# Optimization experiments

Measured on AMD Instinct MI355X. Metric: run time of the kernel, lower is better.

## Reference

```python
import jax, jax.numpy as jnp
import numpy as np

N_NODES = 50000
N_EDGES = 600000
DIMS = [1280, 512, 300, 300]


def setup_inputs() -> dict:
    key = jax.random.key(0)
    ks = jax.random.split(key, 8)
    x = jax.random.normal(ks[0], (N_NODES, DIMS[0]), dtype=jnp.float32)
    edge_index = jax.random.randint(ks[1], (2, N_EDGES), 0, N_NODES, dtype=jnp.int64)
    def w(k, i, o):
        return jax.random.normal(k, (i, o), dtype=jnp.float32) * (1.0 / np.sqrt(i))
    W1 = w(ks[2], DIMS[0], DIMS[1]); b1 = jnp.zeros((DIMS[1],), jnp.float32)
    W2 = w(ks[3], DIMS[1], DIMS[2]); b2 = jnp.zeros((DIMS[2],), jnp.float32)
    W3 = w(ks[4], DIMS[2], DIMS[3]); b3 = jnp.zeros((DIMS[3],), jnp.float32)
    return {"x": x, "W1": W1, "b1": b1, "W2": W2, "b2": b2,
            "W3": W3, "b3": b3, "edge_index": edge_index}


def gcn_conv(x, W, b, src, dst, n):
    """PyG GCNConv: add self-loops, symmetric D^-1/2 (A+I) D^-1/2 aggregation."""
    h = x @ W  # [N, out]
    loops = jnp.arange(n, dtype=src.dtype)
    s = jnp.concatenate([src, loops])  # [E+N]
    d = jnp.concatenate([dst, loops])
    deg = jax.ops.segment_sum(jnp.ones_like(d, dtype=h.dtype), d, num_segments=n)
    dinv = jnp.where(deg > 0, jax.lax.rsqrt(deg), 0.0)
    norm = dinv[s] * dinv[d]  # [E+N]
    out = jax.ops.segment_sum(h[s] * norm[:, None], d, num_segments=n)
    return out + b


def reference(x, W1, b1, W2, b2, W3, b3, edge_index):
    src, dst = edge_index[0], edge_index[1]
    n = x.shape[0]
    # dropout is identity in eval mode; pertubed=False path
    h = jax.nn.relu(gcn_conv(x, W1, b1, src, dst, n))
    h = jax.nn.relu(gcn_conv(h, W2, b2, src, dst, n))
    h = jax.nn.relu(gcn_conv(h, W3, b3, src, dst, n))
    return h  # [N, 300]; per-graph split is a trivial mask over data.batch
```

## Files before the change

### kernel.cpp

```cpp
#include <hip/hip_runtime.h>

typedef _Float16 f16;
typedef _Float16 f16x2 __attribute__((ext_vector_type(2)));
typedef _Float16 f16x4 __attribute__((ext_vector_type(4)));
typedef _Float16 f16x8 __attribute__((ext_vector_type(8)));
typedef float f32x4 __attribute__((ext_vector_type(4)));

#define N_NODES 50000
#define N_EDGES 600000

__device__ __forceinline__ void gl_lds16(const void* g, void* l) {
  __builtin_amdgcn_global_load_lds(
      (__attribute__((address_space(1))) void*)(g),
      (__attribute__((address_space(3))) void*)(l), 16, 0, 0);
}

__global__ void k_setup(const float* __restrict__ x, f16* __restrict__ xh,
                        const float* __restrict__ W1, f16* __restrict__ w1h,
                        const float* __restrict__ W2, f16* __restrict__ w2h,
                        const float* __restrict__ W3, f16* __restrict__ w3h,
                        const float* __restrict__ b2, float* __restrict__ bp2,
                        const float* __restrict__ b3, float* __restrict__ bp3,
                        const int* __restrict__ edst, int* __restrict__ deg) {
  const int b = blockIdx.x, t = threadIdx.x;
  if (b < 62500) {
    long i = (long)b * 256 + t;
    float4 v = ((const float4*)x)[i];
    f16x4 o;
    o[0] = (f16)v.x; o[1] = (f16)v.y; o[2] = (f16)v.z; o[3] = (f16)v.w;
    ((f16x4*)xh)[i] = o;
  } else if (b < 64844) {
    int e = (b - 62500) * 256 + t;
    if (e < N_EDGES) atomicAdd(&deg[edst[e]], 1);
  } else if (b < 67404) {
    int idx = (b - 64844) * 256 + t;
    int n = idx / 1280, k = idx - n * 1280;
    w1h[idx] = (f16)W1[(size_t)k * 512 + n];
  } else if (b < 68004) {
    int bb = b - 67404;
    int n = bb >> 1, k = (bb & 1) * 256 + t;
    if (k < 512) w2h[(size_t)n * 512 + k] = (f16)W2[(size_t)k * 300 + n];
  } else if (b < 68604) {
    int bb = b - 68004;
    int n = bb >> 1, k = (bb & 1) * 256 + t;
    if (k < 320) w3h[(size_t)n * 320 + k] = (k < 300) ? (f16)W3[(size_t)k * 300 + n] : (f16)0.f;
  } else if (b < 68606) {
    int i = (b - 68604) * 256 + t;
    if (i < 320) bp2[i] = (i < 300) ? b2[i] : 0.f;
  } else {
    int i = (b - 68606) * 256 + t;
    if (i < 320) bp3[i] = (i < 300) ? b3[i] : 0.f;
  }
}

__device__ __forceinline__ int block_incl_scan256(int v, int t) {
  __shared__ int wsum[4];
  const int lane = t & 63, w = t >> 6;
  int incl = v;
#pragma unroll
  for (int off = 1; off < 64; off <<= 1) {
    int u = __shfl_up(incl, off, 64);
    if (lane >= off) incl += u;
  }
  if (lane == 63) wsum[w] = incl;
  __syncthreads();
  int add = 0;
#pragma unroll
  for (int k = 0; k < 4; ++k)
    if (k < w) add += wsum[k];
  return incl + add;
}

__global__ void k_scan1(const int* __restrict__ deg, float* __restrict__ dinv,
                        int* __restrict__ bsum, int n) {
  __shared__ int ws4[4];
  const int t = threadIdx.x, b = blockIdx.x;
  const int i = b * 256 + t;
  int v = (i < n) ? deg[i] : 0;
  if (i < n) dinv[i] = rsqrtf((float)(v + 1));
  int s = v;
#pragma unroll
  for (int off = 1; off < 64; off <<= 1) s += __shfl_xor(s, off, 64);
  if ((t & 63) == 0) ws4[t >> 6] = s;
  __syncthreads();
  if (t == 0) bsum[b] = ws4[0] + ws4[1] + ws4[2] + ws4[3];
}

__global__ void k_scan2(const int* __restrict__ bsum, int* __restrict__ bpre,
                        int* __restrict__ rowptr, int nb, int n) {
  const int t = threadIdx.x;
  int v = (t < nb) ? bsum[t] : 0;
  int incl = block_incl_scan256(v, t);
  if (t < nb) bpre[t] = incl - v;
  if (t == 255) rowptr[n] = incl;
}

__global__ void k_scan3(const int* __restrict__ deg, const int* __restrict__ bpre,
                        int* __restrict__ rowptr, int* __restrict__ rptr2, int n) {
  const int t = threadIdx.x, b = blockIdx.x;
  const int i = b * 256 + t;
  int v = (i < n) ? deg[i] : 0;
  int incl = block_incl_scan256(v, t);
  int ex = bpre[b] + incl - v;
  if (i < n) { rowptr[i] = ex; rptr2[i] = ex; }
}

__global__ void k_fill(const int* __restrict__ src, const int* __restrict__ dst,
                       int* __restrict__ rptr2, int2* __restrict__ meta,
                       const float* __restrict__ dinv, int E) {
  int e = blockIdx.x * 256 + threadIdx.x;
  if (e < E) {
    int d = dst[e], s = src[e];
    int pos = atomicAdd(&rptr2[d], 1);
    float w = dinv[s] * dinv[d];
    meta[pos] = make_int2(s, __float_as_int(w));
  }
}

__global__ __launch_bounds__(256, 2)
void gemm_f16_tn(const f16* __restrict__ A, const f16* __restrict__ B,
                 f16* __restrict__ C, int M, int N, int K,
                 int lda, int ldb, int ldc) {
  __shared__ __align__(16) f16 As[128 * 32];
  __shared__ __align__(16) f16 Bs[128 * 32];
  const int tid = threadIdx.x;
  const int wave = tid >> 6;
  const int lane = tid & 63;
  const int bm = blockIdx.x, bn = blockIdx.y;

  const int srow = tid >> 2;
  const int sunit = (tid & 3) ^ ((tid >> 3) & 3);
  long ar0 = (long)bm * 128 + srow;      if (ar0 > M - 1) ar0 = M - 1;
  long ar1 = (long)bm * 128 + srow + 64; if (ar1 > M - 1) ar1 = M - 1;
  long br0 = (long)bn * 128 + srow;      if (br0 > N - 1) br0 = N - 1;
  long br1 = (long)bn * 128 + srow + 64; if (br1 > N - 1) br1 = N - 1;
  const char* aSrc0 = (const char*)(A + ar0 * lda) + sunit * 16;
  const char* aSrc1 = (const char*)(A + ar1 * lda) + sunit * 16;
  const char* bSrc0 = (const char*)(B + br0 * ldb) + sunit * 16;
  const char* bSrc1 = (const char*)(B + br1 * ldb) + sunit * 16;
  char* ldsA0 = (char*)As + wave * 1024;
  char* ldsA1 = (char*)As + 4096 + wave * 1024;
  char* ldsB0 = (char*)Bs + wave * 1024;
  char* ldsB1 = (char*)Bs + 4096 + wave * 1024;

  const int r16 = lane & 15;
  const int kq = lane >> 4;
  const int wm = wave & 1, wn = wave >> 1;

  int aoff[4], boff[4];
#pragma unroll
  for (int t = 0; t < 4; ++t) {
    int arow = wm * 64 + t * 16 + r16;
    aoff[t] = arow * 64 + ((kq ^ ((arow >> 1) & 3)) << 4);
    int brow = wn * 64 + t * 16 + r16;
    boff[t] = brow * 64 + ((kq ^ ((brow >> 1) & 3)) << 4);
  }

  f32x4 acc[4][4] = {};

  for (int k0 = 0; k0 < K; k0 += 32) {
    __syncthreads();
    size_t kb = (size_t)k0 * 2;
    gl_lds16(aSrc0 + kb, ldsA0);
    gl_lds16(aSrc1 + kb, ldsA1);
    gl_lds16(bSrc0 + kb, ldsB0);
    gl_lds16(bSrc1 + kb, ldsB1);
    __syncthreads();

    f16x8 af[4], bf[4];
#pragma unroll
    for (int t = 0; t < 4; ++t) {
      af[t] = *(const f16x8*)((const char*)As + aoff[t]);
      bf[t] = *(const f16x8*)((const char*)Bs + boff[t]);
    }
#pragma unroll
    for (int mt = 0; mt < 4; ++mt)
#pragma unroll
      for (int nt = 0; nt < 4; ++nt)
        acc[mt][nt] = __builtin_amdgcn_mfma_f32_16x16x32_f16(af[mt], bf[nt], acc[mt][nt], 0, 0, 0);
  }

  const int crow0 = bm * 128 + wm * 64;
  const int ccol0 = bn * 128 + wn * 64;
#pragma unroll
  for (int mt = 0; mt < 4; ++mt)
#pragma unroll
    for (int nt = 0; nt < 4; ++nt)
#pragma unroll
      for (int r = 0; r < 4; ++r) {
        int row = crow0 + mt * 16 + kq * 4 + r;
        int col = ccol0 + nt * 16 + r16;
        if (row < M && col < ldc)
          C[(size_t)row * ldc + col] = (col < N) ? (f16)acc[mt][nt][r] : (f16)0.f;
      }
}

template <int LDH, int ACT, bool F16OUT, int DOUT>
__global__ __launch_bounds__(256, 8)
void agg_relu3(const f16* __restrict__ h, const int* __restrict__ rowptr,
               const int2* __restrict__ meta, const float* __restrict__ dinv,
               const float* __restrict__ bias, void* __restrict__ outp, int nNodes) {
  const int tid = threadIdx.x;
  const int lane = tid & 63;
  const int node = blockIdx.x * 4 + (tid >> 6);
  if (node >= nNodes) return;
  const int r0 = __builtin_amdgcn_readfirstlane(rowptr[node]);
  const int r1 = __builtin_amdgcn_readfirstlane(rowptr[node + 1]);
  const float dv = __builtin_bit_cast(
      float, __builtin_amdgcn_readfirstlane(__builtin_bit_cast(int, dinv[node])));

  const int hoff = (lane < ACT ? lane : ACT - 1) * 8;
  const f16* hp = h + hoff;

  float acc[8];
  {
    f16x8 v = *(const f16x8*)(hp + (size_t)node * LDH);
    const float w0 = dv * dv;
#pragma unroll
    for (int j = 0; j < 8; ++j) acc[j] = w0 * (float)v[j];
  }

  for (int base = r0; base < r1; base += 64) {
    const int idx = base + lane;
    int2 m = (idx < r1) ? meta[idx] : make_int2(0, 0);
    const int cnt = min(64, r1 - base);
    int j = 0;
    for (; j + 2 <= cnt; j += 2) {
      int s0 = __shfl(m.x, j, 64);
      int s1 = __shfl(m.x, j + 1, 64);
      float w0 = __int_as_float(__shfl(m.y, j, 64));
      float w1 = __int_as_float(__shfl(m.y, j + 1, 64));
      f16x8 v0 = *(const f16x8*)(hp + (size_t)s0 * LDH);
      f16x8 v1 = *(const f16x8*)(hp + (size_t)s1 * LDH);
#pragma unroll
      for (int q = 0; q < 8; ++q) acc[q] = fmaf(w0, (float)v0[q], acc[q]);
#pragma unroll
      for (int q = 0; q < 8; ++q) acc[q] = fmaf(w1, (float)v1[q], acc[q]);
    }
    if (j < cnt) {
      int s0 = __shfl(m.x, j, 64);
      float w0 = __int_as_float(__shfl(m.y, j, 64));
      f16x8 v0 = *(const f16x8*)(hp + (size_t)s0 * LDH);
#pragma unroll
      for (int q = 0; q < 8; ++q) acc[q] = fmaf(w0, (float)v0[q], acc[q]);
    }
  }

  float4 bv0 = *(const float4*)(bias + hoff);
  float4 bv1 = *(const float4*)(bias + hoff + 4);
  float o[8];
  o[0] = fmaxf(acc[0] + bv0.x, 0.f); o[1] = fmaxf(acc[1] + bv0.y, 0.f);
  o[2] = fmaxf(acc[2] + bv0.z, 0.f); o[3] = fmaxf(acc[3] + bv0.w, 0.f);
  o[4] = fmaxf(acc[4] + bv1.x, 0.f); o[5] = fmaxf(acc[5] + bv1.y, 0.f);
  o[6] = fmaxf(acc[6] + bv1.z, 0.f); o[7] = fmaxf(acc[7] + bv1.w, 0.f);

  if constexpr (F16OUT) {
    if (lane < ACT) {
      f16x8 ov;
#pragma unroll
      for (int j = 0; j < 8; ++j) ov[j] = (f16)o[j];
      *(f16x8*)((f16*)outp + (size_t)node * LDH + lane * 8) = ov;
    }
  } else {
    float* orow = (float*)outp + (size_t)node * DOUT + lane * 8;
    if (lane * 8 + 4 <= DOUT)
      *(float4*)(orow) = make_float4(o[0], o[1], o[2], o[3]);
    if (lane * 8 + 8 <= DOUT)
      *(float4*)(orow + 4) = make_float4(o[4], o[5], o[6], o[7]);
  }
}

extern "C" void kernel_launch(void* const* d_in, const int* in_sizes, int n_in,
                              void* d_out, int out_size, void* d_ws, size_t ws_size,
                              hipStream_t stream) {
  const float* x  = (const float*)d_in[0];
  const float* W1 = (const float*)d_in[1];
  const float* b1 = (const float*)d_in[2];
  const float* W2 = (const float*)d_in[3];
  const float* b2 = (const float*)d_in[4];
  const float* W3 = (const float*)d_in[5];
  const float* b3 = (const float*)d_in[6];
  const int* eidx = (const int*)d_in[7];
  const int* esrc = eidx;
  const int* edst = eidx + N_EDGES;
  float* out = (float*)d_out;

  char* ws = (char*)d_ws;
  f16* xh = (f16*)(ws);
  f16* h2 = (f16*)(ws);
  f16* g2 = (f16*)(ws + 32000000);
  f16* h3 = (f16*)(ws + 64000000);
  f16* h1 = (f16*)(ws + 128000000);
  f16* g1 = (f16*)(ws + 179200000);
  f16* w1h = (f16*)(ws + 230400000);
  f16* w2h = (f16*)(ws + 231710720);
  f16* w3h = (f16*)(ws + 232017920);
  float* bp2 = (float*)(ws + 232209920);
  float* bp3 = (float*)(ws + 232211200);
  int* deg    = (int*)(ws + 232212480);
  float* dinv = (float*)(ws + 232412480);
  int* rowptr = (int*)(ws + 232612480);
  int* rptr2  = (int*)(ws + 232812484);
  int* bsum   = (int*)(ws + 233012488);
  int* bpre   = (int*)(ws + 233013288);
  int2* meta  = (int2*)(ws + 233014088);

  hipMemsetAsync(deg, 0, N_NODES * sizeof(int), stream);

  k_setup<<<68608, 256, 0, stream>>>(x, xh, W1, w1h, W2, w2h, W3, w3h,
                                     b2, bp2, b3, bp3, edst, deg);

  k_scan1<<<196, 256, 0, stream>>>(deg, dinv, bsum, N_NODES);
  k_scan2<<<1, 256, 0, stream>>>(bsum, bpre, rowptr, 196, N_NODES);
  k_scan3<<<196, 256, 0, stream>>>(deg, bpre, rowptr, rptr2, N_NODES);
  k_fill<<<2344, 256, 0, stream>>>(esrc, edst, rptr2, meta, dinv, N_EDGES);

  gemm_f16_tn<<<dim3(391, 4), 256, 0, stream>>>(xh, w1h, h1, N_NODES, 512, 1280, 1280, 1280, 512);
  agg_relu3<512, 64, true, 0><<<12500, 256, 0, stream>>>(h1, rowptr, meta, dinv, b1, g1, N_NODES);

  gemm_f16_tn<<<dim3(391, 3), 256, 0, stream>>>(g1, w2h, h2, N_NODES, 300, 512, 512, 512, 320);
  agg_relu3<320, 40, true, 0><<<12500, 256, 0, stream>>>(h2, rowptr, meta, dinv, bp2, g2, N_NODES);

  gemm_f16_tn<<<dim3(391, 3), 256, 0, stream>>>(g2, w3h, h3, N_NODES, 300, 320, 320, 320, 320);
  agg_relu3<320, 38, false, 300><<<12500, 256, 0, stream>>>(h3, rowptr, meta, dinv, bp3, out, N_NODES);
}
```

Before: 814.1 us.

## Fuse graph CSR build into cooperative kernel and unroll aggregation by four

New measurement: 1.218 ms. 1.5x slower.

```diff
diff --git a/kernel.cpp b/kernel.cpp
--- a/kernel.cpp
+++ b/kernel.cpp
@@ -1,7 +1,9 @@
 #include <hip/hip_runtime.h>
+#include <hip/hip_cooperative_groups.h>
+
+namespace cg = cooperative_groups;
 
 typedef _Float16 f16;
-typedef _Float16 f16x2 __attribute__((ext_vector_type(2)));
 typedef _Float16 f16x4 __attribute__((ext_vector_type(4)));
 typedef _Float16 f16x8 __attribute__((ext_vector_type(8)));
 typedef float f32x4 __attribute__((ext_vector_type(4)));
@@ -21,7 +23,7 @@
                         const float* __restrict__ W3, f16* __restrict__ w3h,
                         const float* __restrict__ b2, float* __restrict__ bp2,
                         const float* __restrict__ b3, float* __restrict__ bp3,
-                        const int* __restrict__ edst, int* __restrict__ deg) {
+                        int* __restrict__ deg) {
   const int b = blockIdx.x, t = threadIdx.x;
   if (b < 62500) {
     long i = (long)b * 256 + t;
@@ -29,32 +31,31 @@
     f16x4 o;
     o[0] = (f16)v.x; o[1] = (f16)v.y; o[2] = (f16)v.z; o[3] = (f16)v.w;
     ((f16x4*)xh)[i] = o;
-  } else if (b < 64844) {
-    int e = (b - 62500) * 256 + t;
-    if (e < N_EDGES) atomicAdd(&deg[edst[e]], 1);
-  } else if (b < 67404) {
-    int idx = (b - 64844) * 256 + t;
+  } else if (b < 65060) {
+    int idx = (b - 62500) * 256 + t;
     int n = idx / 1280, k = idx - n * 1280;
     w1h[idx] = (f16)W1[(size_t)k * 512 + n];
-  } else if (b < 68004) {
-    int bb = b - 67404;
+  } else if (b < 65660) {
+    int bb = b - 65060;
     int n = bb >> 1, k = (bb & 1) * 256 + t;
     if (k < 512) w2h[(size_t)n * 512 + k] = (f16)W2[(size_t)k * 300 + n];
-  } else if (b < 68604) {
-    int bb = b - 68004;
+  } else if (b < 66260) {
+    int bb = b - 65660;
     int n = bb >> 1, k = (bb & 1) * 256 + t;
     if (k < 320) w3h[(size_t)n * 320 + k] = (k < 300) ? (f16)W3[(size_t)k * 300 + n] : (f16)0.f;
-  } else if (b < 68606) {
-    int i = (b - 68604) * 256 + t;
+  } else if (b < 66262) {
+    int i = (b - 66260) * 256 + t;
     if (i < 320) bp2[i] = (i < 300) ? b2[i] : 0.f;
+  } else if (b < 66264) {
+    int i = (b - 66262) * 256 + t;
+    if (i < 320) bp3[i] = (i < 300) ? b3[i] : 0.f;
   } else {
-    int i = (b - 68606) * 256 + t;
-    if (i < 320) bp3[i] = (i < 300) ? b3[i] : 0.f;
-  }
-}
-
-__device__ __forceinline__ int block_incl_scan256(int v, int t) {
-  __shared__ int wsum[4];
+    int i = (b - 66264) * 256 + t;
+    if (i < N_NODES) deg[i] = 0;
+  }
+}
+
+__device__ __forceinline__ int block_incl_scan256(int v, int t, int* wsum) {
   const int lane = t & 63, w = t >> 6;
   int incl = v;
 #pragma unroll
@@ -71,53 +72,62 @@
   return incl + add;
 }
 
-__global__ void k_scan1(const int* __restrict__ deg, float* __restrict__ dinv,
-                        int* __restrict__ bsum, int n) {
-  __shared__ int ws4[4];
+#define GB_BLOCKS 1024
+__global__ __launch_bounds__(256, 4)
+void k_graph(const int* __restrict__ esrc, const int* __restrict__ edst,
+             int* __restrict__ deg, float* __restrict__ dinv,
+             int* __restrict__ rowptr, int* __restrict__ rptr2,
+             int* __restrict__ bsum, int* __restrict__ bpre,
+             int2* __restrict__ meta) {
+  cg::grid_group grid = cg::this_grid();
+  __shared__ int wsum[4];
   const int t = threadIdx.x, b = blockIdx.x;
-  const int i = b * 256 + t;
-  int v = (i < n) ? deg[i] : 0;
-  if (i < n) dinv[i] = rsqrtf((float)(v + 1));
-  int s = v;
-#pragma unroll
-  for (int off = 1; off < 64; off <<= 1) s += __shfl_xor(s, off, 64);
-  if ((t & 63) == 0) ws4[t >> 6] = s;
-  __syncthreads();
-  if (t == 0) bsum[b] = ws4[0] + ws4[1] + ws4[2] + ws4[3];
-}
-
-__global__ void k_scan2(const int* __restrict__ bsum, int* __restrict__ bpre,
-                        int* __restrict__ rowptr, int nb, int n) {
-  const int t = threadIdx.x;
-  int v = (t < nb) ? bsum[t] : 0;
-  int incl = block_incl_scan256(v, t);
-  if (t < nb) bpre[t] = incl - v;
-  if (t == 255) rowptr[n] = incl;
-}
-
-__global__ void k_scan3(const int* __restrict__ deg, const int* __restrict__ bpre,
-                        int* __restrict__ rowptr, int* __restrict__ rptr2, int n) {
-  const int t = threadIdx.x, b = blockIdx.x;
-  const int i = b * 256 + t;
-  int v = (i < n) ? deg[i] : 0;
-  int incl = block_incl_scan256(v, t);
-  int ex = bpre[b] + incl - v;
-  if (i < n) { rowptr[i] = ex; rptr2[i] = ex; }
-}
-
-__global__ void k_fill(const int* __restrict__ src, const int* __restrict__ dst,
-                       int* __restrict__ rptr2, int2* __restrict__ meta,
-                       const float* __restrict__ dinv, int E) {
-  int e = blockIdx.x * 256 + threadIdx.x;
-  if (e < E) {
-    int d = dst[e], s = src[e];
+  const int gtid = b * 256 + t;
+  const int gstride = GB_BLOCKS * 256;
+
+  for (int e = gtid; e < N_EDGES; e += gstride)
+    atomicAdd(&deg[edst[e]], 1);
+  grid.sync();
+
+  if (b < 196) {
+    const int i = gtid;
+    int v = (i < N_NODES) ? deg[i] : 0;
+    if (i < N_NODES) dinv[i] = rsqrtf((float)(v + 1));
+    int s = v;
+#pragma unroll
+    for (int off = 1; off < 64; off <<= 1) s += __shfl_xor(s, off, 64);
+    if ((t & 63) == 0) wsum[t >> 6] = s;
+    __syncthreads();
+    if (t == 0) bsum[b] = wsum[0] + wsum[1] + wsum[2] + wsum[3];
+  }
+  grid.sync();
+
+  if (b == 0) {
+    int v = (t < 196) ? bsum[t] : 0;
+    int incl = block_incl_scan256(v, t, wsum);
+    if (t < 196) bpre[t] = incl - v;
+    if (t == 255) rowptr[N_NODES] = incl;
+  }
+  grid.sync();
+
+  if (b < 196) {
+    const int i = gtid;
+    int v = (i < N_NODES) ? deg[i] : 0;
+    int incl = block_incl_scan256(v, t, wsum);
+    int ex = bpre[b] + incl - v;
+    if (i < N_NODES) { rowptr[i] = ex; rptr2[i] = ex; }
+  }
+  grid.sync();
+
+  for (int e = gtid; e < N_EDGES; e += gstride) {
+    int d = edst[e], s = esrc[e];
     int pos = atomicAdd(&rptr2[d], 1);
     float w = dinv[s] * dinv[d];
     meta[pos] = make_int2(s, __float_as_int(w));
   }
 }
 
-__global__ __launch_bounds__(256, 2)
+__global__ __launch_bounds__(256, 3)
 void gemm_f16_tn(const f16* __restrict__ A, const f16* __restrict__ B,
                  f16* __restrict__ C, int M, int N, int K,
                  int lda, int ldb, int ldc) {
@@ -197,7 +207,7 @@
 
 template <int LDH, int ACT, bool F16OUT, int DOUT>
 __global__ __launch_bounds__(256, 8)
-void agg_relu3(const f16* __restrict__ h, const int* __restrict__ rowptr,
+void agg_relu4(const f16* __restrict__ h, const int* __restrict__ rowptr,
                const int2* __restrict__ meta, const float* __restrict__ dinv,
                const float* __restrict__ bias, void* __restrict__ outp, int nNodes) {
   const int tid = threadIdx.x;
@@ -225,19 +235,29 @@
     int2 m = (idx < r1) ? meta[idx] : make_int2(0, 0);
     const int cnt = min(64, r1 - base);
     int j = 0;
-    for (; j + 2 <= cnt; j += 2) {
+    for (; j + 4 <= cnt; j += 4) {
       int s0 = __shfl(m.x, j, 64);
       int s1 = __shfl(m.x, j + 1, 64);
+      int s2 = __shfl(m.x, j + 2, 64);
+      int s3 = __shfl(m.x, j + 3, 64);
       float w0 = __int_as_float(__shfl(m.y, j, 64));
       float w1 = __int_as_float(__shfl(m.y, j + 1, 64));
+      float w2 = __int_as_float(__shfl(m.y, j + 2, 64));
+      float w3 = __int_as_float(__shfl(m.y, j + 3, 64));
       f16x8 v0 = *(const f16x8*)(hp + (size_t)s0 * LDH);
       f16x8 v1 = *(const f16x8*)(hp + (size_t)s1 * LDH);
+      f16x8 v2 = *(const f16x8*)(hp + (size_t)s2 * LDH);
+      f16x8 v3 = *(const f16x8*)(hp + (size_t)s3 * LDH);
 #pragma unroll
       for (int q = 0; q < 8; ++q) acc[q] = fmaf(w0, (float)v0[q], acc[q]);
 #pragma unroll
       for (int q = 0; q < 8; ++q) acc[q] = fmaf(w1, (float)v1[q], acc[q]);
+#pragma unroll
+      for (int q = 0; q < 8; ++q) acc[q] = fmaf(w2, (float)v2[q], acc[q]);
+#pragma unroll
+      for (int q = 0; q < 8; ++q) acc[q] = fmaf(w3, (float)v3[q], acc[q]);
     }
-    if (j < cnt) {
+    for (; j < cnt; ++j) {
       int s0 = __shfl(m.x, j, 64);
       float w0 = __int_as_float(__shfl(m.y, j, 64));
       f16x8 v0 = *(const f16x8*)(hp + (size_t)s0 * LDH);
@@ -305,22 +325,23 @@
   int* bpre   = (int*)(ws + 233013288);
   int2* meta  = (int2*)(ws + 233014088);
 
-  hipMemsetAsync(deg, 0, N_NODES * sizeof(int), stream);
-
-  k_setup<<<68608, 256, 0, stream>>>(x, xh, W1, w1h, W2, w2h, W3, w3h,
-                                     b2, bp2, b3, bp3, edst, deg);
-
-  k_scan1<<<196, 256, 0, stream>>>(deg, dinv, bsum, N_NODES);
-  k_scan2<<<1, 256, 0, stream>>>(bsum, bpre, rowptr, 196, N_NODES);
-  k_scan3<<<196, 256, 0, stream>>>(deg, bpre, rowptr, rptr2, N_NODES);
-  k_fill<<<2344, 256, 0, stream>>>(esrc, edst, rptr2, meta, dinv, N_EDGES);
+  k_setup<<<66460, 256, 0, stream>>>(x, xh, W1, w1h, W2, w2h, W3, w3h,
+                                     b2, bp2, b3, bp3, deg);
+
+  {
+    void* args[] = {(void*)&esrc, (void*)&edst, (void*)&deg, (void*)&dinv,
+                    (void*)&rowptr, (void*)&rptr2, (void*)&bsum, (void*)&bpre,
+                    (void*)&meta};
+    hipLaunchCooperativeKernel((const void*)k_graph, dim3(GB_BLOCKS), dim3(256),
+                               args, 0, stream);
+  }
 
   gemm_f16_tn<<<dim3(391, 4), 256, 0, stream>>>(xh, w1h, h1, N_NODES, 512, 1280, 1280, 1280, 512);
-  agg_relu3<512, 64, true, 0><<<12500, 256, 0, stream>>>(h1, rowptr, meta, dinv, b1, g1, N_NODES);
+  agg_relu4<512, 64, true, 0><<<12500, 256, 0, stream>>>(h1, rowptr, meta, dinv, b1, g1, N_NODES);
 
   gemm_f16_tn<<<dim3(391, 3), 256, 0, stream>>>(g1, w2h, h2, N_NODES, 300, 512, 512, 512, 320);
-  agg_relu3<320, 40, true, 0><<<12500, 256, 0, stream>>>(h2, rowptr, meta, dinv, bp2, g2, N_NODES);
+  agg_relu4<320, 40, true, 0><<<12500, 256, 0, stream>>>(h2, rowptr, meta, dinv, bp2, g2, N_NODES);
 
   gemm_f16_tn<<<dim3(391, 3), 256, 0, stream>>>(g2, w3h, h3, N_NODES, 300, 320, 320, 320, 320);
-  agg_relu3<320, 38, false, 300><<<12500, 256, 0, stream>>>(h3, rowptr, meta, dinv, bp3, out, N_NODES);
-}
+  agg_relu4<320, 38, false, 300><<<12500, 256, 0, stream>>>(h3, rowptr, meta, dinv, bp3, out, N_NODES);
+}
```
